# Kernel tuning notes

Hardware: AMD Instinct MI355X
Metric: run time of the kernel (lower is better)

The kernel has to match this reference:

```python
import jax, jax.numpy as jnp
import numpy as np

B, L, D = 2, 2048, 2560
H, KV, HD = 8, 4, 256
FF = 10240
WINDOW = 1024
ROPE_BASE = 10000.0
EPS = 1e-6


def rmsnorm(x, scale=None):
    x32 = x.astype(jnp.float32)
    var = jnp.mean(jnp.square(x32), axis=-1, keepdims=True)
    xn = x32 * jax.lax.rsqrt(var + EPS)
    return xn if scale is None else xn * scale.astype(jnp.float32)


def apply_rope(x, positions, base):
    # full RoPE (rope_fraction=1.0): rotate pairs (i, i+head_dim//2)
    hd = x.shape[-1]
    half = hd // 2
    timescale = base ** (2.0 * jnp.arange(half, dtype=jnp.float32) / hd)
    ang = positions[:, :, None].astype(jnp.float32) / timescale  # [B,L,half]
    sin = jnp.sin(ang)[:, :, None, :]  # [B,L,1,half]
    cos = jnp.cos(ang)[:, :, None, :]
    x1, x2 = x[..., :half], x[..., half:]
    return jnp.concatenate([x1 * cos - x2 * sin, x2 * cos + x1 * sin], axis=-1)


def setup_inputs() -> dict:
    key = jax.random.key(0)
    ks = jax.random.split(key, 16)
    s = lambda fan_in: 1.0 / np.sqrt(fan_in)
    return {
        "x": jax.random.normal(ks[0], (B, L, D), jnp.float32),
        "positions": jnp.broadcast_to(jnp.arange(L, dtype=jnp.int32), (B, L)),
        "wq": jax.random.normal(ks[1], (D, H * HD), jnp.float32) * s(D),
        "wk": jax.random.normal(ks[2], (D, KV * HD), jnp.float32) * s(D),
        "wv": jax.random.normal(ks[3], (D, KV * HD), jnp.float32) * s(D),
        "wo": jax.random.normal(ks[4], (H * HD, D), jnp.float32) * s(H * HD),
        "q_scale": jnp.ones((HD,), jnp.float32),
        "k_scale": jnp.ones((HD,), jnp.float32),
        "pre_attn_scale": jnp.ones((D,), jnp.float32),
        "post_attn_scale": jnp.ones((D,), jnp.float32),
        "pre_ffw_scale": jnp.ones((D,), jnp.float32),
        "post_ffw_scale": jnp.ones((D,), jnp.float32),
        "w_gate": jax.random.normal(ks[5], (D, FF), jnp.float32) * s(D),
        "w_up": jax.random.normal(ks[6], (D, FF), jnp.float32) * s(D),
        "w_down": jax.random.normal(ks[7], (FF, D), jnp.float32) * s(FF),
    }


def reference(x, positions, wq, wk, wv, wo, q_scale, k_scale,
              pre_attn_scale, post_attn_scale, pre_ffw_scale, post_ffw_scale,
              w_gate, w_up, w_down):
    # --- attention sub-block ---
    h = rmsnorm(x, pre_attn_scale)
    q = (h @ wq).reshape(B, L, H, HD)
    k = (h @ wk).reshape(B, L, KV, HD)
    v = (h @ wv).reshape(B, L, KV, HD)
    q = apply_rope(rmsnorm(q, q_scale), positions, ROPE_BASE)
    k = apply_rope(rmsnorm(k, k_scale), positions, ROPE_BASE)
    v = rmsnorm(v)  # RMSNormNoScale on V
    rep = H // KV
    k = jnp.repeat(k, rep, axis=2)  # [B,L,H,HD]
    v = jnp.repeat(v, rep, axis=2)
    scores = jnp.einsum("bqhd,bkhd->bhqk", q, k)  # NOTE: no 1/sqrt(d) scaling, faithful to source
    i = jnp.arange(L)[:, None]
    j = jnp.arange(L)[None, :]
    mask = (j <= i) & (j > i - WINDOW)  # causal & sliding window
    scores = jnp.where(mask[None, None, :, :], scores, -10000.0)
    probs = jax.nn.softmax(scores.astype(jnp.float32), axis=-1)
    attn = jnp.einsum("bhqk,bkhd->bqhd", probs, v).reshape(B, L, H * HD)
    attn = attn @ wo
    x = x + rmsnorm(attn, post_attn_scale)
    # --- feedforward sub-block (GeGLU) ---
    h = rmsnorm(x, pre_ffw_scale)
    hidden = jax.nn.gelu(h @ w_gate, approximate=False) * (h @ w_up)
    ffw = hidden @ w_down
    x = x + rmsnorm(ffw, post_ffw_scale)
    return x
```

## Files before the change

### kernel.cpp

```cpp
#include <hip/hip_runtime.h>
#include <math.h>

#define DEV __device__ __forceinline__

typedef _Float16 f16;
typedef _Float16 f16x8 __attribute__((ext_vector_type(8)));
typedef _Float16 f16x4 __attribute__((ext_vector_type(4)));
typedef float f32x4 __attribute__((ext_vector_type(4)));

DEV void gload_lds16(const void* g, void* l) {
  __builtin_amdgcn_global_load_lds(
      (const __attribute__((address_space(1))) void*)g,
      (__attribute__((address_space(3))) void*)l, 16, 0, 0);
}

__global__ __launch_bounds__(256) void transpose_w64(
    const float* __restrict__ src, f16* __restrict__ dst, int R, int C) {
  __shared__ float tile[64][65];
  const int r0 = blockIdx.y * 64, c0 = blockIdx.x * 64;
  const int tid = threadIdx.x;
  const int rr = tid >> 4;
  const int rc = (tid & 15) * 4;
#pragma unroll
  for (int p = 0; p < 4; ++p) {
    int r = p * 16 + rr;
    float4 v = *(const float4*)(src + (size_t)(r0 + r) * C + c0 + rc);
    tile[r][rc] = v.x; tile[r][rc + 1] = v.y;
    tile[r][rc + 2] = v.z; tile[r][rc + 3] = v.w;
  }
  __syncthreads();
  const int wc = tid >> 3;
  const int wk = (tid & 7) * 8;
#pragma unroll
  for (int p = 0; p < 2; ++p) {
    int c = p * 32 + wc;
    f16x8 o;
#pragma unroll
    for (int i = 0; i < 8; ++i) o[i] = (f16)tile[wk + i][c];
    *(f16x8*)(dst + (size_t)(c0 + c) * R + r0 + wk) = o;
  }
}

__global__ void rope_table_k(float* __restrict__ tab) {
  int idx = blockIdx.x * 256 + threadIdx.x;
  int pos = idx >> 7, j = idx & 127;
  float ts = powf(10000.0f, (float)j * (1.0f / 128.0f));
  float ang = (float)pos / ts;
  tab[pos * 256 + j] = sinf(ang);
  tab[pos * 256 + 128 + j] = cosf(ang);
}

__global__ __launch_bounds__(256) void rmsnorm_f32_f16(
    const float* __restrict__ in, const float* __restrict__ scale,
    f16* __restrict__ out) {
  constexpr int D = 2560, N4 = D / 4;
  const int m = blockIdx.x, tid = threadIdx.x;
  const float* row = in + (size_t)m * D;
  float vals[12];
  float ss = 0.f;
#pragma unroll
  for (int it = 0; it < 3; ++it) {
    int c4 = tid + it * 256;
    if (c4 < N4) {
      float4 v = *(const float4*)(row + c4 * 4);
      vals[it * 4 + 0] = v.x; vals[it * 4 + 1] = v.y;
      vals[it * 4 + 2] = v.z; vals[it * 4 + 3] = v.w;
      ss += v.x * v.x + v.y * v.y + v.z * v.z + v.w * v.w;
    }
  }
#pragma unroll
  for (int off = 32; off; off >>= 1) ss += __shfl_xor(ss, off, 64);
  __shared__ float red[4];
  if ((tid & 63) == 0) red[tid >> 6] = ss;
  __syncthreads();
  float rs = rsqrtf((red[0] + red[1] + red[2] + red[3]) * (1.0f / D) + 1e-6f);
#pragma unroll
  for (int it = 0; it < 3; ++it) {
    int c4 = tid + it * 256;
    if (c4 < N4) {
      float4 sc = *(const float4*)(scale + c4 * 4);
      f16x4 o;
      o[0] = (f16)(vals[it * 4 + 0] * rs * sc.x);
      o[1] = (f16)(vals[it * 4 + 1] * rs * sc.y);
      o[2] = (f16)(vals[it * 4 + 2] * rs * sc.z);
      o[3] = (f16)(vals[it * 4 + 3] * rs * sc.w);
      *(f16x4*)(out + (size_t)m * D + c4 * 4) = o;
    }
  }
}

__global__ __launch_bounds__(256) void residual_rmsnorm3(
    const float* __restrict__ x, const f16* __restrict__ y0,
    const f16* __restrict__ y1, const f16* __restrict__ y2,
    const float* __restrict__ scale, float* __restrict__ out,
    const float* __restrict__ scale2, f16* __restrict__ h) {
  constexpr int D = 2560, N4 = D / 4;
  const int m = blockIdx.x, tid = threadIdx.x;
  const size_t base = (size_t)m * D;
  __shared__ float red[4];
  float yv[12];
  float ss = 0.f;
#pragma unroll
  for (int it = 0; it < 3; ++it) {
    int c4 = tid + it * 256;
    if (c4 < N4) {
      f16x4 u = *(const f16x4*)(y0 + base + c4 * 4);
      float a = (float)u[0], b = (float)u[1], c = (float)u[2], d = (float)u[3];
      if (y1) {
        f16x4 v = *(const f16x4*)(y1 + base + c4 * 4);
        f16x4 w2 = *(const f16x4*)(y2 + base + c4 * 4);
        a += (float)v[0] + (float)w2[0]; b += (float)v[1] + (float)w2[1];
        c += (float)v[2] + (float)w2[2]; d += (float)v[3] + (float)w2[3];
      }
      yv[it * 4 + 0] = a; yv[it * 4 + 1] = b; yv[it * 4 + 2] = c; yv[it * 4 + 3] = d;
      ss += a * a + b * b + c * c + d * d;
    }
  }
#pragma unroll
  for (int off = 32; off; off >>= 1) ss += __shfl_xor(ss, off, 64);
  if ((tid & 63) == 0) red[tid >> 6] = ss;
  __syncthreads();
  float rs = rsqrtf((red[0] + red[1] + red[2] + red[3]) * (1.0f / D) + 1e-6f);
  float ss2 = 0.f;
#pragma unroll
  for (int it = 0; it < 3; ++it) {
    int c4 = tid + it * 256;
    if (c4 < N4) {
      float4 xv = *(const float4*)(x + base + c4 * 4);
      float4 sc = *(const float4*)(scale + c4 * 4);
      float4 o;
      o.x = xv.x + yv[it * 4 + 0] * rs * sc.x;
      o.y = xv.y + yv[it * 4 + 1] * rs * sc.y;
      o.z = xv.z + yv[it * 4 + 2] * rs * sc.z;
      o.w = xv.w + yv[it * 4 + 3] * rs * sc.w;
      *(float4*)(out + base + c4 * 4) = o;
      yv[it * 4 + 0] = o.x; yv[it * 4 + 1] = o.y;
      yv[it * 4 + 2] = o.z; yv[it * 4 + 3] = o.w;
      ss2 += o.x * o.x + o.y * o.y + o.z * o.z + o.w * o.w;
    }
  }
  if (h) {
#pragma unroll
    for (int off = 32; off; off >>= 1) ss2 += __shfl_xor(ss2, off, 64);
    __syncthreads();
    if ((tid & 63) == 0) red[tid >> 6] = ss2;
    __syncthreads();
    float rs2 = rsqrtf((red[0] + red[1] + red[2] + red[3]) * (1.0f / D) + 1e-6f);
#pragma unroll
    for (int it = 0; it < 3; ++it) {
      int c4 = tid + it * 256;
      if (c4 < N4) {
        float4 sc = *(const float4*)(scale2 + c4 * 4);
        f16x4 o;
        o[0] = (f16)(yv[it * 4 + 0] * rs2 * sc.x);
        o[1] = (f16)(yv[it * 4 + 1] * rs2 * sc.y);
        o[2] = (f16)(yv[it * 4 + 2] * rs2 * sc.z);
        o[3] = (f16)(yv[it * 4 + 3] * rs2 * sc.w);
        *(f16x4*)(h + base + c4 * 4) = o;
      }
    }
  }
}

__global__ __launch_bounds__(256) void norm_rope_k(
    const f16* __restrict__ qkv, const int* __restrict__ positions,
    const float* __restrict__ q_scale, const float* __restrict__ k_scale,
    const float* __restrict__ tab,
    f16* __restrict__ q_g, f16* __restrict__ k_g, f16* __restrict__ v_n) {
  const int m = blockIdx.x;
  const int tid = threadIdx.x, w = tid >> 6, l = tid & 63;
  const int pos = positions[m];
  const float* srow = tab + (size_t)pos * 256;
  const int c0 = l * 4;
  for (int vi = w; vi < 16; vi += 4) {
    f16x4 u = *(const f16x4*)(qkv + (size_t)m * 4096 + vi * 256 + c0);
    float x0 = (float)u[0], x1 = (float)u[1], x2 = (float)u[2], x3 = (float)u[3];
    float ss = x0 * x0 + x1 * x1 + x2 * x2 + x3 * x3;
#pragma unroll
    for (int off = 32; off; off >>= 1) ss += __shfl_xor(ss, off, 64);
    float rs = rsqrtf(ss * (1.0f / 256.0f) + 1e-6f);
    if (vi < 12) {
      const float* sc = (vi < 8) ? q_scale : k_scale;
      float4 s4 = *(const float4*)(sc + c0);
      float n0 = x0 * rs * s4.x, n1 = x1 * rs * s4.y;
      float n2 = x2 * rs * s4.z, n3 = x3 * rs * s4.w;
      float p0 = __shfl_xor(n0, 32, 64), p1 = __shfl_xor(n1, 32, 64);
      float p2 = __shfl_xor(n2, 32, 64), p3 = __shfl_xor(n3, 32, 64);
      int j0 = c0 & 127;
      float4 sn = *(const float4*)(srow + j0);
      float4 cs = *(const float4*)(srow + 128 + j0);
      float sgn = (l < 32) ? -1.0f : 1.0f;
      f16x4 o;
      o[0] = (f16)(n0 * cs.x + sgn * p0 * sn.x);
      o[1] = (f16)(n1 * cs.y + sgn * p1 * sn.y);
      o[2] = (f16)(n2 * cs.z + sgn * p2 * sn.z);
      o[3] = (f16)(n3 * cs.w + sgn * p3 * sn.w);
      if (vi < 8) *(f16x4*)(q_g + (size_t)m * 2048 + vi * 256 + c0) = o;
      else        *(f16x4*)(k_g + (size_t)m * 1024 + (vi - 8) * 256 + c0) = o;
    } else {
      f16x4 o;
      o[0] = (f16)(x0 * rs); o[1] = (f16)(x1 * rs);
      o[2] = (f16)(x2 * rs); o[3] = (f16)(x3 * rs);
      *(f16x4*)(v_n + (size_t)m * 1024 + (vi - 12) * 256 + c0) = o;
    }
  }
}

__global__ void transpose_v_k(const f16* __restrict__ v_n, f16* __restrict__ vt) {
  __shared__ f16 tile[32][33];
  int bkv = blockIdx.z;
  int b = bkv >> 2, kv = bkv & 3;
  int t0 = blockIdx.x * 32, d0 = blockIdx.y * 32;
  int tx = threadIdx.x, ty = threadIdx.y;
#pragma unroll
  for (int j = 0; j < 32; j += 8)
    tile[ty + j][tx] =
        v_n[(size_t)(b * 2048 + t0 + ty + j) * 1024 + kv * 256 + d0 + tx];
  __syncthreads();
#pragma unroll
  for (int j = 0; j < 32; j += 8)
    vt[((size_t)bkv * 256 + d0 + ty + j) * 2048 + t0 + tx] = tile[tx][ty + j];
}

template <int EPI>
__global__ __launch_bounds__(512, 2) void gemm256(
    const f16* __restrict__ A, const f16* __restrict__ BT,
    f16* __restrict__ C, f16* __restrict__ aux, int M, int N, int K,
    int kt0, int ktn) {
  extern __shared__ __align__(16) f16 lds[];
  const int tid = threadIdx.x;
  const int w = tid >> 6, l = tid & 63;
  const int l15 = l & 15, lk = l >> 4;
  const int wm = w >> 2, wn = w & 3;

  const int orig = blockIdx.y * gridDim.x + blockIdx.x;
  const int bm = orig & 15;
  int bn, sK = 0;
  if constexpr (EPI == 4) {
    const int nper = (((int)(gridDim.x * gridDim.y)) >> 4) / 3;
    const int q = orig >> 4;
    bn = q % nper; sK = q / nper;
  } else {
    bn = orig >> 4;
  }
  int kt0v, ktnv;
  if constexpr (EPI == 4) {
    const int qt = ktn / 3, r = ktn % 3;
    ktnv = qt + (sK < r ? 1 : 0);
    kt0v = sK * qt + (sK < r ? sK : r);
  } else {
    kt0v = kt0; ktnv = ktn;
  }
  const int NT = ktnv;

  const int srow = tid >> 2;
  const int sg = (tid & 3) ^ ((srow >> 1) & 3);
  const f16* pA1 = A + (size_t)(bm * 256 + srow) * K + sg * 8 + kt0v * 64;
  const f16* pA2 = pA1 + (size_t)128 * K;
  const f16* pB1;
  const f16* pB2;
  if constexpr (EPI == 3) {
    pB1 = BT + (size_t)(bn * 128 + srow) * K + sg * 8 + kt0v * 64;
    pB2 = aux + (size_t)(bn * 128 + srow) * K + sg * 8 + kt0v * 64;
  } else {
    pB1 = BT + (size_t)(bn * 256 + srow) * K + sg * 8 + kt0v * 64;
    pB2 = pB1 + (size_t)128 * K;
  }

  auto stage = [&](int op, int kh, int buf, int kt) {
    const int kb = kt * 64 + kh * 32;
    const f16* s1 = (op ? pB1 : pA1) + kb;
    const f16* s2 = (op ? pB2 : pA2) + kb;
    f16* dst = lds + ((buf << 2) + (kh << 1) + op) * 8192 + tid * 8;
    gload_lds16(s1, dst);
    gload_lds16(s2, dst + 4096);
  };

  const int fcol = (lk ^ ((l15 >> 1) & 3)) << 3;
  const int aoff = (wm * 128 + l15) * 32 + fcol;
  const int boff = 8192 + (wn * 64 + l15) * 32 + fcol;

  f32x4 acc[8][4] = {};

  stage(0, 0, 0, 0);
  stage(1, 0, 0, 0);
  stage(0, 1, 0, 0);
  stage(1, 1, 0, 0);
  if (NT > 1) stage(0, 0, 1, 1);
  asm volatile("s_waitcnt vmcnt(6)" ::: "memory");
  __builtin_amdgcn_s_barrier();
  asm volatile("" ::: "memory");

  for (int t = 0; t < NT; ++t) {
    const int buf = t & 1, nbuf = buf ^ 1;
    const f16* lb0 = lds + buf * 32768;
    const f16* lb1 = lb0 + 16384;
    {
      f16x8 a1[4], b[4], a2[4];
#pragma unroll
      for (int i = 0; i < 4; ++i) a1[i] = *(const f16x8*)(lb0 + aoff + i * 512);
#pragma unroll
      for (int i = 0; i < 4; ++i) b[i] = *(const f16x8*)(lb0 + boff + i * 512);
#pragma unroll
      for (int i = 0; i < 4; ++i) a2[i] = *(const f16x8*)(lb0 + aoff + (4 + i) * 512);
      if (t + 1 < NT) stage(1, 0, nbuf, t + 1);
      __builtin_amdgcn_s_setprio(1);
#pragma unroll
      for (int mi = 0; mi < 4; ++mi)
#pragma unroll
        for (int ni = 0; ni < 4; ++ni)
          acc[mi][ni] = __builtin_amdgcn_mfma_f32_16x16x32_f16(a1[mi], b[ni], acc[mi][ni], 0, 0, 0);
      __builtin_amdgcn_s_setprio(0);
      if (t + 1 < NT) stage(0, 1, nbuf, t + 1);
      __builtin_amdgcn_s_setprio(1);
#pragma unroll
      for (int mi = 0; mi < 4; ++mi)
#pragma unroll
        for (int ni = 0; ni < 4; ++ni)
          acc[4 + mi][ni] = __builtin_amdgcn_mfma_f32_16x16x32_f16(a2[mi], b[ni], acc[4 + mi][ni], 0, 0, 0);
      __builtin_amdgcn_s_setprio(0);
    }
    if (t + 1 < NT) asm volatile("s_waitcnt vmcnt(6)" ::: "memory");
    else            asm volatile("s_waitcnt vmcnt(0)" ::: "memory");
    __builtin_amdgcn_s_barrier();
    asm volatile("" ::: "memory");
    {
      f16x8 a1[4], b[4], a2[4];
#pragma unroll
      for (int i = 0; i < 4; ++i) a1[i] = *(const f16x8*)(lb1 + aoff + i * 512);
#pragma unroll
      for (int i = 0; i < 4; ++i) b[i] = *(const f16x8*)(lb1 + boff + i * 512);
#pragma unroll
      for (int i = 0; i < 4; ++i) a2[i] = *(const f16x8*)(lb1 + aoff + (4 + i) * 512);
      if (t + 1 < NT) stage(1, 1, nbuf, t + 1);
      __builtin_amdgcn_s_setprio(1);
#pragma unroll
      for (int mi = 0; mi < 4; ++mi)
#pragma unroll
        for (int ni = 0; ni < 4; ++ni)
          acc[mi][ni] = __builtin_amdgcn_mfma_f32_16x16x32_f16(a1[mi], b[ni], acc[mi][ni], 0, 0, 0);
      __builtin_amdgcn_s_setprio(0);
      if (t + 2 < NT) stage(0, 0, buf, t + 2);
      __builtin_amdgcn_s_setprio(1);
#pragma unroll
      for (int mi = 0; mi < 4; ++mi)
#pragma unroll
        for (int ni = 0; ni < 4; ++ni)
          acc[4 + mi][ni] = __builtin_amdgcn_mfma_f32_16x16x32_f16(a2[mi], b[ni], acc[4 + mi][ni], 0, 0, 0);
      __builtin_amdgcn_s_setprio(0);
    }
    if (t + 2 < NT)      asm volatile("s_waitcnt vmcnt(6)" ::: "memory");
    else if (t + 1 < NT) asm volatile("s_waitcnt vmcnt(4)" ::: "memory");
    else                 asm volatile("s_waitcnt vmcnt(0)" ::: "memory");
    __builtin_amdgcn_s_barrier();
    asm volatile("" ::: "memory");
  }

  if constexpr (EPI == 3) {
    constexpr int XP = 136;
    __syncthreads();
    f16* xls = lds;
    if (wn < 2) {
#pragma unroll
      for (int mi = 0; mi < 8; ++mi)
#pragma unroll
        for (int ni = 0; ni < 4; ++ni)
#pragma unroll
          for (int i = 0; i < 4; ++i) {
            int row = wm * 128 + mi * 16 + lk * 4 + i;
            int col = wn * 64 + ni * 16 + l15;
            float v = acc[mi][ni][i];
            v = 0.5f * v * (1.0f + erff(v * 0.70710678118654752f));
            xls[row * XP + col] = (f16)v;
          }
    }
    __syncthreads();
    if (wn >= 2) {
#pragma unroll
      for (int mi = 0; mi < 8; ++mi)
#pragma unroll
        for (int ni = 0; ni < 4; ++ni)
#pragma unroll
          for (int i = 0; i < 4; ++i) {
            int row = wm * 128 + mi * 16 + lk * 4 + i;
            int colg = (wn - 2) * 64 + ni * 16 + l15;
            float g = (float)xls[row * XP + colg];
            float v = g * acc[mi][ni][i];
            C[(size_t)(bm * 256 + row) * N + bn * 128 + colg] = (f16)v;
          }
    }
  } else {
    f16* Co = C;
    if constexpr (EPI == 4) {
      if (sK) Co = aux + (size_t)(sK - 1) * ((size_t)M * N);
    }
#pragma unroll
    for (int mi = 0; mi < 8; ++mi) {
#pragma unroll
      for (int ni = 0; ni < 4; ++ni) {
#pragma unroll
        for (int i = 0; i < 4; ++i) {
          int row = bm * 256 + wm * 128 + mi * 16 + lk * 4 + i;
          int col = bn * 256 + wn * 64 + ni * 16 + l15;
          size_t idx = (size_t)row * N + col;
          float v = acc[mi][ni][i];
          if constexpr (EPI == 1) {
            v = 0.5f * v * (1.0f + erff(v * 0.70710678118654752f));
          } else if constexpr (EPI == 2) {
            v *= (float)aux[idx];
          }
          Co[idx] = (f16)v;
        }
      }
    }
  }
}

__global__ __launch_bounds__(256) void flash_attn_k(
    const f16* __restrict__ q_g, const f16* __restrict__ k_g,
    const f16* __restrict__ vt, f16* __restrict__ ctx) {
  constexpr int KP = 264, VP = 40, PP = 40;
  __shared__ f16 Ks[32 * KP];
  __shared__ f16 Vs[256 * VP];
  __shared__ f16 Ps[4][16 * PP];
  const int qt = blockIdx.x, h = blockIdx.y, b = blockIdx.z;
  const int tid = threadIdx.x, w = tid >> 6, l = tid & 63;
  const int l15 = l & 15, lk = l >> 4;
  const int kv = h >> 1;

  f16x8 aq[8];
  const int qrow = qt * 64 + w * 16 + l15;
  const f16* qp = q_g + (size_t)(b * 2048 + qrow) * 2048 + h * 256 + lk * 8;
#pragma unroll
  for (int kc = 0; kc < 8; ++kc) aq[kc] = *(const f16x8*)(qp + kc * 32);

  f32x4 o[16] = {};
  float mrow[4] = {-1e30f, -1e30f, -1e30f, -1e30f};
  float lrow[4] = {0.f, 0.f, 0.f, 0.f};

  int kt_lo = 2 * qt - 32; if (kt_lo < 0) kt_lo = 0;
  const int kt_hi = 2 * qt + 1;
  const int iqb = qt * 64 + w * 16 + lk * 4;

  for (int kt = kt_lo; kt <= kt_hi; ++kt) {
    __syncthreads();
#pragma unroll
    for (int it = 0; it < 4; ++it) {
      int ch = tid + it * 256;
      int jl = ch >> 5, kcc = (ch & 31) * 8;
      *(f16x8*)&Ks[jl * KP + kcc] = *(const f16x8*)(
          k_g + (size_t)(b * 2048 + kt * 32 + jl) * 1024 + kv * 256 + kcc);
      int d = ch >> 2, tc = (ch & 3) * 8;
      *(f16x8*)&Vs[d * VP + tc] = *(const f16x8*)(
          vt + ((size_t)(b * 4 + kv) * 256 + d) * 2048 + kt * 32 + tc);
    }
    __syncthreads();
    f32x4 s[2] = {};
#pragma unroll
    for (int ct = 0; ct < 2; ++ct)
#pragma unroll
      for (int kc = 0; kc < 8; ++kc) {
        f16x8 bk = *(const f16x8*)&Ks[(ct * 16 + l15) * KP + kc * 32 + lk * 8];
        s[ct] = __builtin_amdgcn_mfma_f32_16x16x32_f16(aq[kc], bk, s[ct], 0, 0, 0);
      }
    float pm[4] = {-1e30f, -1e30f, -1e30f, -1e30f};
#pragma unroll
    for (int ct = 0; ct < 2; ++ct)
#pragma unroll
      for (int i = 0; i < 4; ++i) {
        int iq = iqb + i;
        int j = kt * 32 + ct * 16 + l15;
        bool valid = (j <= iq) && (j > iq - 1024);
        float sv = valid ? s[ct][i] : -1e30f;
        s[ct][i] = sv;
        pm[i] = fmaxf(pm[i], sv);
      }
#pragma unroll
    for (int i = 0; i < 4; ++i)
#pragma unroll
      for (int off = 1; off < 16; off <<= 1)
        pm[i] = fmaxf(pm[i], __shfl_xor(pm[i], off, 64));
    float corr[4], rsum[4];
#pragma unroll
    for (int i = 0; i < 4; ++i) {
      float mn = fmaxf(mrow[i], pm[i]);
      corr[i] = __expf(mrow[i] - mn);
      mrow[i] = mn;
      rsum[i] = 0.f;
    }
#pragma unroll
    for (int ct = 0; ct < 2; ++ct)
#pragma unroll
      for (int i = 0; i < 4; ++i) {
        float p = (s[ct][i] > -1e29f) ? __expf(s[ct][i] - mrow[i]) : 0.f;
        s[ct][i] = p;
        rsum[i] += p;
      }
#pragma unroll
    for (int i = 0; i < 4; ++i) {
#pragma unroll
      for (int off = 1; off < 16; off <<= 1) rsum[i] += __shfl_xor(rsum[i], off, 64);
      lrow[i] = lrow[i] * corr[i] + rsum[i];
    }
#pragma unroll
    for (int dt = 0; dt < 16; ++dt)
#pragma unroll
      for (int i = 0; i < 4; ++i) o[dt][i] *= corr[i];
#pragma unroll
    for (int ct = 0; ct < 2; ++ct)
#pragma unroll
      for (int i = 0; i < 4; ++i)
        Ps[w][(lk * 4 + i) * PP + ct * 16 + l15] = (f16)s[ct][i];
    __syncthreads();
    f16x8 pa = *(const f16x8*)&Ps[w][l15 * PP + lk * 8];
#pragma unroll
    for (int dt = 0; dt < 16; ++dt) {
      f16x8 bv = *(const f16x8*)&Vs[(dt * 16 + l15) * VP + lk * 8];
      o[dt] = __builtin_amdgcn_mfma_f32_16x16x32_f16(pa, bv, o[dt], 0, 0, 0);
    }
  }
  float inv[4];
#pragma unroll
  for (int i = 0; i < 4; ++i) inv[i] = 1.0f / lrow[i];
  f16* op = ctx + (size_t)(b * 2048 + qt * 64 + w * 16 + lk * 4) * 2048 + h * 256 + l15;
#pragma unroll
  for (int dt = 0; dt < 16; ++dt)
#pragma unroll
    for (int i = 0; i < 4; ++i)
      op[(size_t)i * 2048 + dt * 16] = (f16)(o[dt][i] * inv[i]);
}

extern "C" void kernel_launch(void* const* d_in, const int* in_sizes, int n_in,
                              void* d_out, int out_size, void* d_ws, size_t ws_size,
                              hipStream_t stream) {
  const float* x = (const float*)d_in[0];
  const int* positions = (const int*)d_in[1];
  const float* wq = (const float*)d_in[2];
  const float* wk = (const float*)d_in[3];
  const float* wv = (const float*)d_in[4];
  const float* wo = (const float*)d_in[5];
  const float* q_scale = (const float*)d_in[6];
  const float* k_scale = (const float*)d_in[7];
  const float* pre_attn = (const float*)d_in[8];
  const float* post_attn = (const float*)d_in[9];
  const float* pre_ffw = (const float*)d_in[10];
  const float* post_ffw = (const float*)d_in[11];
  const float* w_gate = (const float*)d_in[12];
  const float* w_up = (const float*)d_in[13];
  const float* w_down = (const float*)d_in[14];
  float* out = (float*)d_out;

  static bool s_attr = []() {
    hipFuncSetAttribute(reinterpret_cast<const void*>(&gemm256<0>),
                        hipFuncAttributeMaxDynamicSharedMemorySize, 131072);
    hipFuncSetAttribute(reinterpret_cast<const void*>(&gemm256<1>),
                        hipFuncAttributeMaxDynamicSharedMemorySize, 131072);
    hipFuncSetAttribute(reinterpret_cast<const void*>(&gemm256<2>),
                        hipFuncAttributeMaxDynamicSharedMemorySize, 131072);
    hipFuncSetAttribute(reinterpret_cast<const void*>(&gemm256<3>),
                        hipFuncAttributeMaxDynamicSharedMemorySize, 131072);
    hipFuncSetAttribute(reinterpret_cast<const void*>(&gemm256<4>),
                        hipFuncAttributeMaxDynamicSharedMemorySize, 131072);
    return true;
  }();
  (void)s_attr;

  const size_t WT_BIG   = (size_t)20480 * 2560 * 2;
  const size_t WT_SMALL = (size_t)10240 * 2560 * 2;
  const size_t TAB_B = (size_t)2048 * 256 * 4;
  const size_t H_B   = (size_t)4096 * 2560 * 2;
  const size_t ACT_B = (size_t)92280832;
  auto aln = [](size_t v) { return (v + 255) & ~(size_t)255; };
  const bool big = ws_size >= aln(WT_BIG) + aln(TAB_B) + aln(H_B) + aln(ACT_B);

  char* ws = (char*)d_ws;
  size_t off = 0;
  auto alloc = [&](size_t bytes) {
    char* p = ws + off;
    off += (bytes + 255) & ~(size_t)255;
    return p;
  };
  f16* wT    = (f16*)alloc(big ? WT_BIG : WT_SMALL);
  float* tab = (float*)alloc(TAB_B);
  f16* h     = (f16*)alloc(H_B);
  char* act  = alloc(ACT_B);
  f16* qkv    = (f16*)(act);
  f16* q_g    = (f16*)(act + (size_t)33554432);
  f16* k_g    = (f16*)(act + (size_t)33554432 + 16777216);
  f16* v_n    = (f16*)(act + (size_t)33554432 + 16777216 + 8388608);
  f16* vtb    = (f16*)(act + (size_t)33554432 + 16777216 + 2 * 8388608);
  f16* ctx    = (f16*)(act + (size_t)33554432 + 16777216 + 3 * 8388608);
  f16* attn_o = (f16*)(act);
  f16* gbuf = (f16*)(act);
  f16* ffw  = h;
  f16* wuT  = wT + (size_t)10240 * 2560;
  f16* ap1  = wuT;
  f16* fp1  = wT;
  (void)in_sizes; (void)n_in; (void)out_size;

  rope_table_k<<<1024, 256, 0, stream>>>(tab);

  rmsnorm_f32_f16<<<4096, 256, 0, stream>>>(x, pre_attn, h);
  transpose_w64<<<dim3(2048 / 64, 2560 / 64), 256, 0, stream>>>(wq, wT, 2560, 2048);
  transpose_w64<<<dim3(1024 / 64, 2560 / 64), 256, 0, stream>>>(wk, wT + (size_t)2048 * 2560, 2560, 1024);
  transpose_w64<<<dim3(1024 / 64, 2560 / 64), 256, 0, stream>>>(wv, wT + (size_t)3072 * 2560, 2560, 1024);
  gemm256<0><<<dim3(16, 16), 512, 131072, stream>>>(h, wT, qkv, nullptr, 4096, 4096, 2560, 0, 40);
  norm_rope_k<<<4096, 256, 0, stream>>>(qkv, positions, q_scale, k_scale, tab, q_g, k_g, v_n);
  transpose_v_k<<<dim3(2048 / 32, 256 / 32, 8), dim3(32, 8), 0, stream>>>(v_n, vtb);
  flash_attn_k<<<dim3(32, 8, 2), 256, 0, stream>>>(q_g, k_g, vtb, ctx);
  transpose_w64<<<dim3(2560 / 64, 2048 / 64), 256, 0, stream>>>(wo, wT, 2048, 2560);
  if (big) {
    gemm256<4><<<dim3(30, 16), 512, 131072, stream>>>(ctx, wT, attn_o, ap1, 4096, 2560, 2048, 0, 32);
    residual_rmsnorm3<<<4096, 256, 0, stream>>>(x, attn_o, ap1, ap1 + (size_t)4096 * 2560,
                                                post_attn, out, pre_ffw, h);
  } else {
    gemm256<0><<<dim3(10, 16), 512, 131072, stream>>>(ctx, wT, attn_o, nullptr, 4096, 2560, 2048, 0, 32);
    residual_rmsnorm3<<<4096, 256, 0, stream>>>(x, attn_o, nullptr, nullptr,
                                                post_attn, out, pre_ffw, h);
  }

  if (big) {
    transpose_w64<<<dim3(10240 / 64, 2560 / 64), 256, 0, stream>>>(w_gate, wT, 2560, 10240);
    transpose_w64<<<dim3(10240 / 64, 2560 / 64), 256, 0, stream>>>(w_up, wuT, 2560, 10240);
    gemm256<3><<<dim3(80, 16), 512, 131072, stream>>>(h, wT, gbuf, wuT, 4096, 10240, 2560, 0, 40);
    transpose_w64<<<dim3(2560 / 64, 10240 / 64), 256, 0, stream>>>(w_down, wuT, 10240, 2560);
    gemm256<4><<<dim3(30, 16), 512, 131072, stream>>>(gbuf, wuT, ffw, fp1, 4096, 2560, 10240, 0, 160);
    residual_rmsnorm3<<<4096, 256, 0, stream>>>(out, ffw, fp1, fp1 + (size_t)4096 * 2560,
                                                post_ffw, out, nullptr, nullptr);
  } else {
    transpose_w64<<<dim3(10240 / 64, 2560 / 64), 256, 0, stream>>>(w_gate, wT, 2560, 10240);
    gemm256<1><<<dim3(40, 16), 512, 131072, stream>>>(h, wT, gbuf, nullptr, 4096, 10240, 2560, 0, 40);
    transpose_w64<<<dim3(10240 / 64, 2560 / 64), 256, 0, stream>>>(w_up, wT, 2560, 10240);
    gemm256<2><<<dim3(40, 16), 512, 131072, stream>>>(h, wT, gbuf, gbuf, 4096, 10240, 2560, 0, 40);
    transpose_w64<<<dim3(2560 / 64, 10240 / 64), 256, 0, stream>>>(w_down, wT, 10240, 2560);
    gemm256<0><<<dim3(10, 16), 512, 131072, stream>>>(gbuf, wT, ffw, nullptr, 4096, 2560, 10240, 0, 160);
    residual_rmsnorm3<<<4096, 256, 0, stream>>>(out, ffw, nullptr, nullptr,
                                                post_ffw, out, nullptr, nullptr);
  }
}
```

Baseline: 1.154 ms.

## Switch GEMM to triple-buffered 32-wide K stages with register-level GeGLU epilogue

Restructures the gemm256 main loop from double-buffered 64-wide K tiles (two half-steps each) into a three-stage ring of 32-wide K tiles, with one barrier per step and prefetch two stages ahead. LDS use drops from 128KB to 96KB. The GeGLU variant now interleaves gate and up columns per wave, so the gelu*up product is computed in registers without the LDS exchange and extra syncs. The cost is twice as many loop iterations and barriers, plus a fix to include kt0 in the split-K start offset.

Measured after the change: 1.092 ms (median of 2 runs). 1.06x faster.

```diff
diff --git a/kernel.cpp b/kernel.cpp
--- a/kernel.cpp
+++ b/kernel.cpp
@@ -247,7 +247,7 @@
   if constexpr (EPI == 4) {
     const int qt = ktn / 3, r = ktn % 3;
     ktnv = qt + (sK < r ? 1 : 0);
-    kt0v = sK * qt + (sK < r ? sK : r);
+    kt0v = kt0 + sK * qt + (sK < r ? sK : r);
   } else {
     kt0v = kt0; ktnv = ktn;
   }
@@ -255,140 +255,96 @@
 
   const int srow = tid >> 2;
   const int sg = (tid & 3) ^ ((srow >> 1) & 3);
-  const f16* pA1 = A + (size_t)(bm * 256 + srow) * K + sg * 8 + kt0v * 64;
-  const f16* pA2 = pA1 + (size_t)128 * K;
-  const f16* pB1;
-  const f16* pB2;
+  const f16* src0 = A + (size_t)(bm * 256 + srow) * K + sg * 8 + kt0v * 32;
+  const f16* src1 = src0 + (size_t)128 * K;
+  const f16* src2;
+  const f16* src3;
   if constexpr (EPI == 3) {
-    pB1 = BT + (size_t)(bn * 128 + srow) * K + sg * 8 + kt0v * 64;
-    pB2 = aux + (size_t)(bn * 128 + srow) * K + sg * 8 + kt0v * 64;
-  } else {
-    pB1 = BT + (size_t)(bn * 256 + srow) * K + sg * 8 + kt0v * 64;
-    pB2 = pB1 + (size_t)128 * K;
-  }
-
-  auto stage = [&](int op, int kh, int buf, int kt) {
-    const int kb = kt * 64 + kh * 32;
-    const f16* s1 = (op ? pB1 : pA1) + kb;
-    const f16* s2 = (op ? pB2 : pA2) + kb;
-    f16* dst = lds + ((buf << 2) + (kh << 1) + op) * 8192 + tid * 8;
-    gload_lds16(s1, dst);
-    gload_lds16(s2, dst + 4096);
+    src2 = BT + (size_t)(bn * 128 + srow) * K + sg * 8 + kt0v * 32;
+    src3 = aux + (size_t)(bn * 128 + srow) * K + sg * 8 + kt0v * 32;
+  } else {
+    src2 = BT + (size_t)(bn * 256 + srow) * K + sg * 8 + kt0v * 32;
+    src3 = src2 + (size_t)128 * K;
+  }
+
+  auto stage = [&](int buf, int kt) {
+    f16* base = lds + buf * 16384 + tid * 8;
+    const int kb = kt * 32;
+    gload_lds16(src0 + kb, base);
+    gload_lds16(src1 + kb, base + 4096);
+    gload_lds16(src2 + kb, base + 8192);
+    gload_lds16(src3 + kb, base + 12288);
   };
 
   const int fcol = (lk ^ ((l15 >> 1) & 3)) << 3;
-  const int aoff = (wm * 128 + l15) * 32 + fcol;
-  const int boff = 8192 + (wn * 64 + l15) * 32 + fcol;
+  const int aoff = wm * 4096 + l15 * 32 + fcol;
+  int boff;
+  if constexpr (EPI != 3) {
+    boff = (2 + (wn >> 1)) * 4096 + ((wn & 1) * 64 + l15) * 32 + fcol;
+  } else {
+    boff = 8192 + (wn * 32 + l15) * 32 + fcol;
+  }
 
   f32x4 acc[8][4] = {};
 
-  stage(0, 0, 0, 0);
-  stage(1, 0, 0, 0);
-  stage(0, 1, 0, 0);
-  stage(1, 1, 0, 0);
-  if (NT > 1) stage(0, 0, 1, 1);
-  asm volatile("s_waitcnt vmcnt(6)" ::: "memory");
+  stage(0, 0);
+  if (NT > 1) {
+    stage(1, 1);
+    asm volatile("s_waitcnt vmcnt(4)" ::: "memory");
+  } else {
+    asm volatile("s_waitcnt vmcnt(0)" ::: "memory");
+  }
   __builtin_amdgcn_s_barrier();
   asm volatile("" ::: "memory");
 
+  int buf = 0;
   for (int t = 0; t < NT; ++t) {
-    const int buf = t & 1, nbuf = buf ^ 1;
-    const f16* lb0 = lds + buf * 32768;
-    const f16* lb1 = lb0 + 16384;
-    {
-      f16x8 a1[4], b[4], a2[4];
-#pragma unroll
-      for (int i = 0; i < 4; ++i) a1[i] = *(const f16x8*)(lb0 + aoff + i * 512);
-#pragma unroll
-      for (int i = 0; i < 4; ++i) b[i] = *(const f16x8*)(lb0 + boff + i * 512);
-#pragma unroll
-      for (int i = 0; i < 4; ++i) a2[i] = *(const f16x8*)(lb0 + aoff + (4 + i) * 512);
-      if (t + 1 < NT) stage(1, 0, nbuf, t + 1);
-      __builtin_amdgcn_s_setprio(1);
-#pragma unroll
-      for (int mi = 0; mi < 4; ++mi)
-#pragma unroll
-        for (int ni = 0; ni < 4; ++ni)
-          acc[mi][ni] = __builtin_amdgcn_mfma_f32_16x16x32_f16(a1[mi], b[ni], acc[mi][ni], 0, 0, 0);
-      __builtin_amdgcn_s_setprio(0);
-      if (t + 1 < NT) stage(0, 1, nbuf, t + 1);
-      __builtin_amdgcn_s_setprio(1);
-#pragma unroll
-      for (int mi = 0; mi < 4; ++mi)
-#pragma unroll
-        for (int ni = 0; ni < 4; ++ni)
-          acc[4 + mi][ni] = __builtin_amdgcn_mfma_f32_16x16x32_f16(a2[mi], b[ni], acc[4 + mi][ni], 0, 0, 0);
-      __builtin_amdgcn_s_setprio(0);
-    }
-    if (t + 1 < NT) asm volatile("s_waitcnt vmcnt(6)" ::: "memory");
-    else            asm volatile("s_waitcnt vmcnt(0)" ::: "memory");
-    __builtin_amdgcn_s_barrier();
-    asm volatile("" ::: "memory");
-    {
-      f16x8 a1[4], b[4], a2[4];
-#pragma unroll
-      for (int i = 0; i < 4; ++i) a1[i] = *(const f16x8*)(lb1 + aoff + i * 512);
-#pragma unroll
-      for (int i = 0; i < 4; ++i) b[i] = *(const f16x8*)(lb1 + boff + i * 512);
-#pragma unroll
-      for (int i = 0; i < 4; ++i) a2[i] = *(const f16x8*)(lb1 + aoff + (4 + i) * 512);
-      if (t + 1 < NT) stage(1, 1, nbuf, t + 1);
-      __builtin_amdgcn_s_setprio(1);
-#pragma unroll
-      for (int mi = 0; mi < 4; ++mi)
-#pragma unroll
-        for (int ni = 0; ni < 4; ++ni)
-          acc[mi][ni] = __builtin_amdgcn_mfma_f32_16x16x32_f16(a1[mi], b[ni], acc[mi][ni], 0, 0, 0);
-      __builtin_amdgcn_s_setprio(0);
-      if (t + 2 < NT) stage(0, 0, buf, t + 2);
-      __builtin_amdgcn_s_setprio(1);
-#pragma unroll
-      for (int mi = 0; mi < 4; ++mi)
-#pragma unroll
-        for (int ni = 0; ni < 4; ++ni)
-          acc[4 + mi][ni] = __builtin_amdgcn_mfma_f32_16x16x32_f16(a2[mi], b[ni], acc[4 + mi][ni], 0, 0, 0);
-      __builtin_amdgcn_s_setprio(0);
-    }
-    if (t + 2 < NT)      asm volatile("s_waitcnt vmcnt(6)" ::: "memory");
-    else if (t + 1 < NT) asm volatile("s_waitcnt vmcnt(4)" ::: "memory");
-    else                 asm volatile("s_waitcnt vmcnt(0)" ::: "memory");
-    __builtin_amdgcn_s_barrier();
-    asm volatile("" ::: "memory");
+    const int bb = buf * 16384;
+    f16x8 a[8], b[4];
+#pragma unroll
+    for (int i = 0; i < 8; ++i) a[i] = *(const f16x8*)(lds + bb + aoff + i * 512);
+    if constexpr (EPI == 3) {
+      b[0] = *(const f16x8*)(lds + bb + boff);
+      b[1] = *(const f16x8*)(lds + bb + boff + 512);
+      b[2] = *(const f16x8*)(lds + bb + boff + 4096);
+      b[3] = *(const f16x8*)(lds + bb + boff + 4096 + 512);
+    } else {
+#pragma unroll
+      for (int i = 0; i < 4; ++i) b[i] = *(const f16x8*)(lds + bb + boff + i * 512);
+    }
+    if (t + 2 < NT) {
+      int nb = buf + 2; if (nb >= 3) nb -= 3;
+      stage(nb, t + 2);
+    }
+    __builtin_amdgcn_s_setprio(1);
+#pragma unroll
+    for (int mi = 0; mi < 8; ++mi)
+#pragma unroll
+      for (int ni = 0; ni < 4; ++ni)
+        acc[mi][ni] = __builtin_amdgcn_mfma_f32_16x16x32_f16(a[mi], b[ni], acc[mi][ni], 0, 0, 0);
+    __builtin_amdgcn_s_setprio(0);
+    if (t + 1 < NT) {
+      if (t + 2 < NT) asm volatile("s_waitcnt vmcnt(4)" ::: "memory");
+      else            asm volatile("s_waitcnt vmcnt(0)" ::: "memory");
+      __builtin_amdgcn_s_barrier();
+      asm volatile("" ::: "memory");
+    }
+    ++buf; if (buf >= 3) buf = 0;
   }
 
   if constexpr (EPI == 3) {
-    constexpr int XP = 136;
-    __syncthreads();
-    f16* xls = lds;
-    if (wn < 2) {
-#pragma unroll
-      for (int mi = 0; mi < 8; ++mi)
-#pragma unroll
-        for (int ni = 0; ni < 4; ++ni)
-#pragma unroll
-          for (int i = 0; i < 4; ++i) {
-            int row = wm * 128 + mi * 16 + lk * 4 + i;
-            int col = wn * 64 + ni * 16 + l15;
-            float v = acc[mi][ni][i];
-            v = 0.5f * v * (1.0f + erff(v * 0.70710678118654752f));
-            xls[row * XP + col] = (f16)v;
-          }
-    }
-    __syncthreads();
-    if (wn >= 2) {
-#pragma unroll
-      for (int mi = 0; mi < 8; ++mi)
-#pragma unroll
-        for (int ni = 0; ni < 4; ++ni)
-#pragma unroll
-          for (int i = 0; i < 4; ++i) {
-            int row = wm * 128 + mi * 16 + lk * 4 + i;
-            int colg = (wn - 2) * 64 + ni * 16 + l15;
-            float g = (float)xls[row * XP + colg];
-            float v = g * acc[mi][ni][i];
-            C[(size_t)(bm * 256 + row) * N + bn * 128 + colg] = (f16)v;
-          }
-    }
+#pragma unroll
+    for (int mi = 0; mi < 8; ++mi)
+#pragma unroll
+      for (int ni = 0; ni < 2; ++ni)
+#pragma unroll
+        for (int i = 0; i < 4; ++i) {
+          int row = bm * 256 + wm * 128 + mi * 16 + lk * 4 + i;
+          int col = bn * 128 + wn * 32 + ni * 16 + l15;
+          float g = acc[mi][ni][i];
+          g = 0.5f * g * (1.0f + erff(g * 0.70710678118654752f));
+          C[(size_t)row * N + col] = (f16)(g * acc[mi][ni + 2][i]);
+        }
   } else {
     f16* Co = C;
     if constexpr (EPI == 4) {
@@ -552,15 +508,15 @@
 
   static bool s_attr = []() {
     hipFuncSetAttribute(reinterpret_cast<const void*>(&gemm256<0>),
-                        hipFuncAttributeMaxDynamicSharedMemorySize, 131072);
+                        hipFuncAttributeMaxDynamicSharedMemorySize, 98304);
     hipFuncSetAttribute(reinterpret_cast<const void*>(&gemm256<1>),
-                        hipFuncAttributeMaxDynamicSharedMemorySize, 131072);
+                        hipFuncAttributeMaxDynamicSharedMemorySize, 98304);
     hipFuncSetAttribute(reinterpret_cast<const void*>(&gemm256<2>),
-                        hipFuncAttributeMaxDynamicSharedMemorySize, 131072);
+                        hipFuncAttributeMaxDynamicSharedMemorySize, 98304);
     hipFuncSetAttribute(reinterpret_cast<const void*>(&gemm256<3>),
-                        hipFuncAttributeMaxDynamicSharedMemorySize, 131072);
+                        hipFuncAttributeMaxDynamicSharedMemorySize, 98304);
     hipFuncSetAttribute(reinterpret_cast<const void*>(&gemm256<4>),
-                        hipFuncAttributeMaxDynamicSharedMemorySize, 131072);
+                        hipFuncAttributeMaxDynamicSharedMemorySize, 98304);
     return true;
   }();
   (void)s_attr;
@@ -604,17 +560,17 @@
   transpose_w64<<<dim3(2048 / 64, 2560 / 64), 256, 0, stream>>>(wq, wT, 2560, 2048);
   transpose_w64<<<dim3(1024 / 64, 2560 / 64), 256, 0, stream>>>(wk, wT + (size_t)2048 * 2560, 2560, 1024);
   transpose_w64<<<dim3(1024 / 64, 2560 / 64), 256, 0, stream>>>(wv, wT + (size_t)3072 * 2560, 2560, 1024);
-  gemm256<0><<<dim3(16, 16), 512, 131072, stream>>>(h, wT, qkv, nullptr, 4096, 4096, 2560, 0, 40);
+  gemm256<0><<<dim3(16, 16), 512, 98304, stream>>>(h, wT, qkv, nullptr, 4096, 4096, 2560, 0, 80);
   norm_rope_k<<<4096, 256, 0, stream>>>(qkv, positions, q_scale, k_scale, tab, q_g, k_g, v_n);
   transpose_v_k<<<dim3(2048 / 32, 256 / 32, 8), dim3(32, 8), 0, stream>>>(v_n, vtb);
   flash_attn_k<<<dim3(32, 8, 2), 256, 0, stream>>>(q_g, k_g, vtb, ctx);
   transpose_w64<<<dim3(2560 / 64, 2048 / 64), 256, 0, stream>>>(wo, wT, 2048, 2560);
   if (big) {
-    gemm256<4><<<dim3(30, 16), 512, 131072, stream>>>(ctx, wT, attn_o, ap1, 4096, 2560, 2048, 0, 32);
+    gemm256<4><<<dim3(30, 16), 512, 98304, stream>>>(ctx, wT, attn_o, ap1, 4096, 2560, 2048, 0, 64);
     residual_rmsnorm3<<<4096, 256, 0, stream>>>(x, attn_o, ap1, ap1 + (size_t)4096 * 2560,
                                                 post_attn, out, pre_ffw, h);
   } else {
-    gemm256<0><<<dim3(10, 16), 512, 131072, stream>>>(ctx, wT, attn_o, nullptr, 4096, 2560, 2048, 0, 32);
+    gemm256<0><<<dim3(10, 16), 512, 98304, stream>>>(ctx, wT, attn_o, nullptr, 4096, 2560, 2048, 0, 64);
     residual_rmsnorm3<<<4096, 256, 0, stream>>>(x, attn_o, nullptr, nullptr,
                                                 post_attn, out, pre_ffw, h);
   }
@@ -622,18 +578,18 @@
   if (big) {
     transpose_w64<<<dim3(10240 / 64, 2560 / 64), 256, 0, stream>>>(w_gate, wT, 2560, 10240);
     transpose_w64<<<dim3(10240 / 64, 2560 / 64), 256, 0, stream>>>(w_up, wuT, 2560, 10240);
-    gemm256<3><<<dim3(80, 16), 512, 131072, stream>>>(h, wT, gbuf, wuT, 4096, 10240, 2560, 0, 40);
+    gemm256<3><<<dim3(80, 16), 512, 98304, stream>>>(h, wT, gbuf, wuT, 4096, 10240, 2560, 0, 80);
     transpose_w64<<<dim3(2560 / 64, 10240 / 64), 256, 0, stream>>>(w_down, wuT, 10240, 2560);
-    gemm256<4><<<dim3(30, 16), 512, 131072, stream>>>(gbuf, wuT, ffw, fp1, 4096, 2560, 10240, 0, 160);
+    gemm256<4><<<dim3(30, 16), 512, 98304, stream>>>(gbuf, wuT, ffw, fp1, 4096, 2560, 10240, 0, 320);
     residual_rmsnorm3<<<4096, 256, 0, stream>>>(out, ffw, fp1, fp1 + (size_t)4096 * 2560,
                                                 post_ffw, out, nullptr, nullptr);
   } else {
     transpose_w64<<<dim3(10240 / 64, 2560 / 64), 256, 0, stream>>>(w_gate, wT, 2560, 10240);
-    gemm256<1><<<dim3(40, 16), 512, 131072, stream>>>(h, wT, gbuf, nullptr, 4096, 10240, 2560, 0, 40);
+    gemm256<1><<<dim3(40, 16), 512, 98304, stream>>>(h, wT, gbuf, nullptr, 4096, 10240, 2560, 0, 80);
     transpose_w64<<<dim3(10240 / 64, 2560 / 64), 256, 0, stream>>>(w_up, wT, 2560, 10240);
-    gemm256<2><<<dim3(40, 16), 512, 131072, stream>>>(h, wT, gbuf, gbuf, 4096, 10240, 2560, 0, 40);
+    gemm256<2><<<dim3(40, 16), 512, 98304, stream>>>(h, wT, gbuf, gbuf, 4096, 10240, 2560, 0, 80);
     transpose_w64<<<dim3(2560 / 64, 10240 / 64), 256, 0, stream>>>(w_down, wT, 10240, 2560);
-    gemm256<0><<<dim3(10, 16), 512, 131072, stream>>>(gbuf, wT, ffw, nullptr, 4096, 2560, 10240, 0, 160);
+    gemm256<0><<<dim3(10, 16), 512, 98304, stream>>>(gbuf, wT, ffw, nullptr, 4096, 2560, 10240, 0, 320);
     residual_rmsnorm3<<<4096, 256, 0, stream>>>(out, ffw, nullptr, nullptr,
                                                 post_ffw, out, nullptr, nullptr);
   }
```
